# Performance work log

Measured on AMD Instinct MI355X. Metric: run time of the kernel, lower is better.

The kernel has to match this reference:

```python
import jax, jax.numpy as jnp
import numpy as np
import math

N_HEADS = 16
D_EFF = 64
ROPE_BASE = 500.0


def _rope(x, cos, sin):
    # x: (b, h, L, d_eff); cos/sin: (L, d_eff//2)
    x_even = x[..., 0::2]
    x_odd = x[..., 1::2]
    rot = jnp.stack([x_even * cos - x_odd * sin,
                     x_even * sin + x_odd * cos], axis=-1)
    return rot.reshape(x.shape)


def setup_inputs() -> dict:
    key = jax.random.key(0)
    ks = jax.random.split(key, 5)
    B, L, D = 1, 2048, 1024
    X = jax.random.normal(ks[0], (B, L, D), dtype=jnp.float32)
    # causal mask (1 = keep, 0 = masked), broadcastable to (B, h, L, L)
    mask = jnp.tril(jnp.ones((L, L), dtype=jnp.int32))[None, :, :]
    s = 1.0 / math.sqrt(D)
    Wq = jax.random.normal(ks[1], (D, D), dtype=jnp.float32) * s
    Wk = jax.random.normal(ks[2], (D, D), dtype=jnp.float32) * s
    Wv = jax.random.normal(ks[3], (D, D), dtype=jnp.float32) * s
    Wo = jax.random.normal(ks[4], (D, D), dtype=jnp.float32) * s
    return {"X": X, "mask": mask, "Wq": Wq, "Wk": Wk, "Wv": Wv, "Wo": Wo}


def reference(X, mask, Wq, Wk, Wv, Wo):
    b, L, d_model = X.shape
    h, d = N_HEADS, D_EFF
    d_full = h * d

    def split_heads(Y):
        return Y.reshape(b, L, h, d).transpose(0, 2, 1, 3)  # (b,h,L,d)

    Q = split_heads(X @ Wq)
    K = split_heads(X @ Wk)
    V = split_heads(X @ Wv)

    # interleaved RoPE, base 500
    inv_freq = 1.0 / (ROPE_BASE ** (jnp.arange(0, d, 2, dtype=jnp.float32) / d))
    freqs = jnp.arange(L, dtype=jnp.float32)[:, None] * inv_freq  # (L, d/2)
    cos, sin = jnp.cos(freqs), jnp.sin(freqs)
    Q = _rope(Q, cos, sin)
    K = _rope(K, cos, sin)

    S = jnp.einsum('bhqd,bhkd->bhqk', Q, K) / math.sqrt(d)
    S = jnp.where(mask[:, None, :, :] == 0, jnp.float32(-1e9), S)
    # NOTE: faithful to original torch code: softmax over the HEADS axis (dim=1)
    A = jax.nn.softmax(S, axis=1)
    Y = jnp.einsum('bhqk,bhkd->bhqd', A, V)
    Y = Y.transpose(0, 2, 1, 3).reshape(b, L, d_full)
    Y = Y @ Wo
    return Y * math.sqrt(d_model / d_full)
```

## Files before the change

kernel.cpp:

```cpp
#include <hip/hip_runtime.h>
#include <stdint.h>
#include <stddef.h>
#include <math.h>

typedef __attribute__((ext_vector_type(8))) short bf16x8;
typedef __attribute__((ext_vector_type(4))) short short4v;
typedef __attribute__((ext_vector_type(4))) float f32x4;

__device__ __forceinline__ short f2bf(float f) {
  union { float f; uint32_t u; } x; x.f = f;
  return (short)((x.u + 0x7fffu + ((x.u >> 16) & 1u)) >> 16);
}
__device__ __forceinline__ float bf2f(short s) {
  union { uint32_t u; float f; } x; x.u = ((uint32_t)(uint16_t)s) << 16;
  return x.f;
}
__device__ __forceinline__ uint32_t cvt_pk_bf16(float a, float b) {
  uint32_t r;
  asm("v_cvt_pk_bf16_f32 %0, %1, %2" : "=v"(r) : "v"(a), "v"(b));
  return r;
}

__device__ __forceinline__ void gload_lds16(const void* g, void* lds) {
  __builtin_amdgcn_global_load_lds(
      (const __attribute__((address_space(1))) void*)g,
      (__attribute__((address_space(3))) void*)lds, 16, 0, 0);
}

__global__ __launch_bounds__(256) void cast_b(const float* __restrict__ s,
                                              short* __restrict__ d) {
  int i4 = (blockIdx.x * 256 + threadIdx.x) * 4;
  float4 v = *(const float4*)&s[i4];
  short4v r = { f2bf(v.x), f2bf(v.y), f2bf(v.z), f2bf(v.w) };
  *(short4v*)&d[i4] = r;
}

__global__ __launch_bounds__(256) void reduce_y(const short* __restrict__ Ypc,
                                                const float* __restrict__ Cvs,
                                                short* __restrict__ o) {
  int q = blockIdx.x;
  int j = q >> 5, qr = q & 31;
  int col = threadIdx.x * 4;
  float a0 = Cvs[col + 0], a1 = Cvs[col + 1], a2 = Cvs[col + 2], a3 = Cvs[col + 3];
  int cf = (j - 2) >> 2;
  for (int c = 0; c <= cf; c++) {
    int slot = (c <= 7) ? (c + 8 * (j - 4 * c - 2)) : ((15 - c) + 8 * j);
    const short* p = Ypc + ((size_t)slot * 32 + qr) * 1024 + col;
    short4v v = *(const short4v*)p;
    a0 += bf2f(v[0]); a1 += bf2f(v[1]); a2 += bf2f(v[2]); a3 += bf2f(v[3]);
  }
  if ((j & 3) < 2) {
    int cp = j >> 2;
    int slot = (cp <= 7) ? (cp + 8 * (64 + (j & 3)))
                         : ((15 - cp) + 8 * (66 + (j & 3)));
    const short* p = Ypc + ((size_t)slot * 32 + qr) * 1024 + col;
    short4v v = *(const short4v*)p;
    a0 += bf2f(v[0]); a1 += bf2f(v[1]); a2 += bf2f(v[2]); a3 += bf2f(v[3]);
  }
  uint32_t u0 = cvt_pk_bf16(a0, a1), u1 = cvt_pk_bf16(a2, a3);
  short4v rr = { (short)u0, (short)(u0 >> 16), (short)u1, (short)(u1 >> 16) };
  *(short4v*)&o[(size_t)q * 1024 + col] = rr;
}

__global__ __launch_bounds__(256) void transW(const float* __restrict__ Wq,
                                              const float* __restrict__ Wk,
                                              const float* __restrict__ Wv,
                                              const float* __restrict__ Wo,
                                              short* __restrict__ WcatT,
                                              short* __restrict__ WoT) {
  int z = blockIdx.z;
  const float* src = (z == 0) ? Wq : (z == 1) ? Wk : (z == 2) ? Wv : Wo;
  short* dst = (z == 3) ? WoT : WcatT + (size_t)z * 1024 * 1024;
  __shared__ float tl[32][33];
  int tx = threadIdx.x & 31, ty = threadIdx.x >> 5;
  int kk0 = blockIdx.x * 32;
  int nn0 = blockIdx.y * 32;
#pragma unroll
  for (int j = 0; j < 4; j++)
    tl[ty + j * 8][tx] = src[(size_t)(kk0 + ty + j * 8) * 1024 + nn0 + tx];
  __syncthreads();
#pragma unroll
  for (int j = 0; j < 4; j++)
    dst[(size_t)(nn0 + ty + j * 8) * 1024 + kk0 + tx] = f2bf(tl[tx][ty + j * 8]);
}

__global__ __launch_bounds__(256) void transpose_v(const short* __restrict__ Vb,
                                                   short* __restrict__ Vt) {
  __shared__ short tv[64][72];
  int h = blockIdx.y, k0 = blockIdx.x * 64;
  int tid = threadIdx.x;
#pragma unroll
  for (int j = 0; j < 2; j++) {
    int idx = tid + j * 256;
    int row = idx >> 3, c = idx & 7;
    bf16x8 v = *(const bf16x8*)&Vb[((size_t)h * 2048 + k0 + row) * 64 + c * 8];
#pragma unroll
    for (int t = 0; t < 8; t++) tv[row][c * 8 + t] = v[t];
  }
  __syncthreads();
#pragma unroll
  for (int j = 0; j < 2; j++) {
    int idx = tid + j * 256;
    int d = idx >> 3, c = idx & 7;
    bf16x8 v;
#pragma unroll
    for (int t = 0; t < 8; t++) v[t] = tv[c * 8 + t][d];
    *(bf16x8*)&Vt[((size_t)h * 64 + d) * 2048 + k0 + c * 8] = v;
  }
}

__global__ __launch_bounds__(256) void vsum(const short* __restrict__ Vb,
                                            float* __restrict__ Cvs) {
  __shared__ float red[16][17];
  int h = blockIdx.x >> 2, dq = blockIdx.x & 3;
  int dl = threadIdx.x & 15, ks = threadIdx.x >> 4;
  int d = dq * 16 + dl;
  float acc = 0.f;
  const short* base = &Vb[((size_t)h * 2048 + ks * 128) * 64 + d];
#pragma unroll 8
  for (int k = 0; k < 128; k++) acc += bf2f(base[(size_t)k * 64]);
  red[dl][ks] = acc;
  __syncthreads();
  if (threadIdx.x < 16) {
    float sum = 0.f;
#pragma unroll
    for (int i = 0; i < 16; i++) sum += red[threadIdx.x][i];
    Cvs[h * 64 + dq * 16 + threadIdx.x] = sum * 0.0625f;
  }
}

template <int MODE>
__global__ __launch_bounds__(256, 2)
void gemm_kernel(const short* __restrict__ A, const short* __restrict__ B,
                 int N, int K, float* __restrict__ C,
                 short* __restrict__ Qb, short* __restrict__ Kb,
                 short* __restrict__ Vb) {
  __shared__ __attribute__((aligned(16))) short lga[128 * 64];
  __shared__ __attribute__((aligned(16))) short lgb[128 * 64];
  const int tid = threadIdx.x;
  const int lane = tid & 63;
  const int w = tid >> 6;
  const int l15 = lane & 15;
  const int quad = lane >> 4;
  const int wm = w >> 1, wn = w & 1;
  const int m0 = blockIdx.x * 128, n0 = blockIdx.y * 128;
  const int rsub = lane >> 3;
  const int cpos = lane & 7;

  f32x4 acc[4][4];
#pragma unroll
  for (int i = 0; i < 4; i++)
#pragma unroll
    for (int j = 0; j < 4; j++) acc[i][j] = (f32x4){0.f, 0.f, 0.f, 0.f};

  for (int kb = 0; kb < K; kb += 64) {
    __syncthreads();
#pragma unroll
    for (int j = 0; j < 4; j++) {
      int r = (w * 4 + j) * 8 + rsub;
      int kc = cpos ^ rsub;
      gload_lds16(A + (size_t)(m0 + r) * K + kb + kc * 8, &lga[(w * 4 + j) * 512]);
      gload_lds16(B + (size_t)(n0 + r) * K + kb + kc * 8, &lgb[(w * 4 + j) * 512]);
    }
    __syncthreads();
#pragma unroll
    for (int kk = 0; kk < 2; kk++) {
      bf16x8 af[4], bfr[4];
#pragma unroll
      for (int t = 0; t < 4; t++) {
        int row = wm * 64 + t * 16 + l15;
        int pc = (kk * 4 + quad) ^ (row & 7);
        af[t] = *(const bf16x8*)&lga[row * 64 + pc * 8];
        int rowb = wn * 64 + t * 16 + l15;
        int pcb = (kk * 4 + quad) ^ (rowb & 7);
        bfr[t] = *(const bf16x8*)&lgb[rowb * 64 + pcb * 8];
      }
#pragma unroll
      for (int mt = 0; mt < 4; mt++)
#pragma unroll
        for (int nt = 0; nt < 4; nt++)
          acc[mt][nt] = __builtin_amdgcn_mfma_f32_16x16x32_bf16(
              af[mt], bfr[nt], acc[mt][nt], 0, 0, 0);
    }
  }

  if (MODE == 0) {
#pragma unroll
    for (int mt = 0; mt < 4; mt++) {
      int q = m0 + wm * 64 + mt * 16 + quad * 4;
#pragma unroll
      for (int nt = 0; nt < 4; nt++) {
        int n = n0 + wn * 64 + nt * 16 + l15;
#pragma unroll
        for (int r = 0; r < 4; r++) C[(size_t)(q + r) * N + n] = acc[mt][nt][r];
      }
    }
  } else {
#pragma unroll
    for (int mt = 0; mt < 4; mt++) {
#pragma unroll
      for (int nt = 0; nt < 4; nt++) {
        int n = n0 + wn * 64 + nt * 16 + l15;
        int mat = n >> 10;
        int h = (n >> 6) & 15;
        int d = n & 63;
#pragma unroll
        for (int r = 0; r < 4; r++) {
          int q = m0 + wm * 64 + mt * 16 + quad * 4 + r;
          float v = acc[mt][nt][r];
          float o = __shfl_xor(v, 1, 64);
          if (mat < 2) {
            int i = d >> 1;
            float ang = (float)q * __builtin_exp2f(-(float)i * 0.2801807588956902f);
            float sn, cs;
            __sincosf(ang, &sn, &cs);
            float rv = (d & 1) ? (o * sn + v * cs) : (v * cs - o * sn);
            short* dst = (mat == 0) ? Qb : Kb;
            dst[((size_t)h * 2048 + q) * 64 + d] = f2bf(rv);
          } else {
            Vb[((size_t)h * 2048 + q) * 64 + d] = f2bf(v);
          }
        }
      }
    }
  }
}

__global__ __launch_bounds__(1024, 2)
void attn_kernel(const short* __restrict__ Qb, const short* __restrict__ Kb,
                 const short* __restrict__ Vt, short* __restrict__ Ypc) {
  __shared__ short Sb[16 * 32 * 72];
  const int tid = threadIdx.x;
  const int lane = tid & 63;
  const int h = tid >> 6;
  const int l15 = lane & 15, quad = lane >> 4;
  const int b = blockIdx.x;
  const int x = b & 7, s = b >> 3;
  int c, j, ng;
  const int n1 = 62 - 4 * x;
  if (s < n1)      { c = x;      j = 4 * x + 2 + s;        ng = 2; }
  else if (s < 64) { c = 15 - x; j = s;                    ng = 2; }
  else if (s < 66) { c = x;      j = 4 * x + (s - 64);     ng = 1; }
  else             { c = 15 - x; j = 60 - 4 * x + (s - 66); ng = 1; }
  const int q0 = j * 32;
  const int g0 = 2 * c;

  bf16x8 qf[2][2];
#pragma unroll
  for (int qs = 0; qs < 2; qs++)
#pragma unroll
    for (int cc = 0; cc < 2; cc++)
      qf[qs][cc] = *(const bf16x8*)&Qb[((size_t)h * 2048 + q0 + qs * 16 + l15) * 64 +
                                       cc * 32 + quad * 8];

  f32x4 yacc[2][4];
#pragma unroll
  for (int i = 0; i < 2; i++)
#pragma unroll
    for (int jj = 0; jj < 4; jj++) yacc[i][jj] = (f32x4){0.f, 0.f, 0.f, 0.f};

  for (int gi = 0; gi < ng; gi++) {
    const int k0 = (g0 + gi) * 64;
#pragma unroll
    for (int st = 0; st < 4; st++) {
      const short* kb = &Kb[((size_t)h * 2048 + k0 + st * 16 + l15) * 64 + quad * 8];
      bf16x8 kf0 = *(const bf16x8*)kb;
      bf16x8 kf1 = *(const bf16x8*)(kb + 32);
#pragma unroll
      for (int qs = 0; qs < 2; qs++) {
        f32x4 sa = (f32x4){0.f, 0.f, 0.f, 0.f};
        sa = __builtin_amdgcn_mfma_f32_16x16x32_bf16(qf[qs][0], kf0, sa, 0, 0, 0);
        sa = __builtin_amdgcn_mfma_f32_16x16x32_bf16(qf[qs][1], kf1, sa, 0, 0, 0);
        const float cs = 0.18033688011112042f;
        uint32_t u0 = cvt_pk_bf16(sa[0] * cs, sa[1] * cs);
        uint32_t u1 = cvt_pk_bf16(sa[2] * cs, sa[3] * cs);
        int rb = (h * 32 + qs * 16 + quad * 4) * 72 + st * 16 + l15;
        Sb[rb]       = (short)u0;
        Sb[rb + 72]  = (short)(u0 >> 16);
        Sb[rb + 144] = (short)u1;
        Sb[rb + 216] = (short)(u1 >> 16);
      }
    }
    __syncthreads();
#pragma unroll
    for (int pp = 0; pp < 2; pp++) {
      int p = tid + pp * 1024;
      int q = p >> 6, kl = p & 63;
      int base = q * 72 + kl;
      float t[16];
      float sum = 0.f;
#pragma unroll
      for (int hh = 0; hh < 16; hh++) {
        float e = __builtin_exp2f(bf2f(Sb[hh * 2304 + base]));
        t[hh] = e;
        sum += e;
      }
      bool msk = (k0 + kl) > (q0 + q);
      float rs = msk ? 0.f : 1.f / sum;
      float offv = msk ? 0.f : 0.0625f;
#pragma unroll
      for (int hh = 0; hh < 16; hh += 2) {
        uint32_t u = cvt_pk_bf16(t[hh] * rs - offv, t[hh + 1] * rs - offv);
        Sb[hh * 2304 + base]       = (short)u;
        Sb[(hh + 1) * 2304 + base] = (short)(u >> 16);
      }
    }
    __syncthreads();
#pragma unroll
    for (int kk = 0; kk < 2; kk++) {
      bf16x8 af0 = *(const bf16x8*)&Sb[(h * 32 + l15) * 72 + kk * 32 + quad * 8];
      bf16x8 af1 = *(const bf16x8*)&Sb[(h * 32 + 16 + l15) * 72 + kk * 32 + quad * 8];
#pragma unroll
      for (int nt = 0; nt < 4; nt++) {
        bf16x8 vf = *(const bf16x8*)&Vt[((size_t)h * 64 + nt * 16 + l15) * 2048 +
                                        k0 + kk * 32 + quad * 8];
        yacc[0][nt] = __builtin_amdgcn_mfma_f32_16x16x32_bf16(af0, vf, yacc[0][nt],
                                                              0, 0, 0);
        yacc[1][nt] = __builtin_amdgcn_mfma_f32_16x16x32_bf16(af1, vf, yacc[1][nt],
                                                              0, 0, 0);
      }
    }
    __syncthreads();
  }
  short* Y = Ypc + (size_t)b * 32 * 1024;
#pragma unroll
  for (int qs = 0; qs < 2; qs++) {
#pragma unroll
    for (int nt = 0; nt < 4; nt++) {
      int col = h * 64 + nt * 16 + l15;
#pragma unroll
      for (int rr = 0; rr < 4; rr++)
        Y[(size_t)(qs * 16 + quad * 4 + rr) * 1024 + col] = f2bf(yacc[qs][nt][rr]);
    }
  }
}

extern "C" void kernel_launch(void* const* d_in, const int* in_sizes, int n_in,
                              void* d_out, int out_size, void* d_ws, size_t ws_size,
                              hipStream_t stream) {
  (void)in_sizes; (void)n_in; (void)out_size; (void)ws_size;
  const float* X  = (const float*)d_in[0];
  const float* Wq = (const float*)d_in[2];
  const float* Wk = (const float*)d_in[3];
  const float* Wv = (const float*)d_in[4];
  const float* Wo = (const float*)d_in[5];
  char* ws = (char*)d_ws;
  const size_t MB = 1024 * 1024;
  short* Xbf   = (short*)(ws + 0);
  short* WcatT = (short*)(ws + 4 * MB);
  short* WoT   = (short*)(ws + 10 * MB);
  short* Qb    = (short*)(ws + 12 * MB);
  short* Kb    = (short*)(ws + 16 * MB);
  short* Vb    = (short*)(ws + 20 * MB);
  short* Vt    = (short*)(ws + 24 * MB);
  short* Ypc   = (short*)(ws + 28 * MB);
  float* Cvs   = (float*)(ws + 63 * MB);
  short* Ycbf  = Xbf;
  float* out   = (float*)d_out;

  cast_b<<<dim3(2048), dim3(256), 0, stream>>>(X, Xbf);
  transW<<<dim3(32, 32, 4), dim3(256), 0, stream>>>(Wq, Wk, Wv, Wo, WcatT, WoT);
  gemm_kernel<1><<<dim3(16, 24), dim3(256), 0, stream>>>(Xbf, WcatT, 3072, 1024,
                                                         nullptr, Qb, Kb, Vb);
  transpose_v<<<dim3(32, 16), dim3(256), 0, stream>>>(Vb, Vt);
  vsum<<<dim3(64), dim3(256), 0, stream>>>(Vb, Cvs);
  attn_kernel<<<dim3(544), dim3(1024), 0, stream>>>(Qb, Kb, Vt, Ypc);
  reduce_y<<<dim3(2048), dim3(256), 0, stream>>>(Ypc, Cvs, Ycbf);
  gemm_kernel<0><<<dim3(16, 8), dim3(256), 0, stream>>>(Ycbf, WoT, 1024, 1024,
                                                        out, nullptr, nullptr, nullptr);
}
```

Before: 212.3 us.

## Double-buffer attention score tiles and regroup work into 288 larger blocks

The attention kernel now gives each block up to four 64-key groups instead of two, which cuts the grid from 544 to 288 blocks and shrinks the partial-sum reduction. It uses two LDS score buffers so the PV MFMAs of the previous group overlap the QK of the next, and raises wave priority during PV. Softmax handles two key columns per thread with 32-bit LDS accesses. Doubling LDS and setting launch bounds to one block per CU lowers occupancy, and fewer, longer blocks can leave CUs unevenly loaded.

```diff
diff --git a/kernel.cpp b/kernel.cpp
--- a/kernel.cpp
+++ b/kernel.cpp
@@ -42,19 +42,16 @@
   int j = q >> 5, qr = q & 31;
   int col = threadIdx.x * 4;
   float a0 = Cvs[col + 0], a1 = Cvs[col + 1], a2 = Cvs[col + 2], a3 = Cvs[col + 3];
-  int cf = (j - 2) >> 2;
-  for (int c = 0; c <= cf; c++) {
-    int slot = (c <= 7) ? (c + 8 * (j - 4 * c - 2)) : ((15 - c) + 8 * j);
-    const short* p = Ypc + ((size_t)slot * 32 + qr) * 1024 + col;
-    short4v v = *(const short4v*)p;
-    a0 += bf2f(v[0]); a1 += bf2f(v[1]); a2 += bf2f(v[2]); a3 += bf2f(v[3]);
-  }
-  if ((j & 3) < 2) {
-    int cp = j >> 2;
-    int slot = (cp <= 7) ? (cp + 8 * (64 + (j & 3)))
-                         : ((15 - cp) + 8 * (66 + (j & 3)));
-    const short* p = Ypc + ((size_t)slot * 32 + qr) * 1024 + col;
-    short4v v = *(const short4v*)p;
+  int cmax = j >> 3;
+  for (int c = 0; c <= cmax; c++) {
+    int p, t;
+    if (c < 4) { p = c;     t = j - 8 * c; }
+    else       { p = 7 - c; t = j + 8; }
+    int x = 2 * p + (t & 1);
+    int s = 35 - (t >> 1);
+    int slot = x + 8 * s;
+    const short* pp = Ypc + ((size_t)slot * 32 + qr) * 1024 + col;
+    short4v v = *(const short4v*)pp;
     a0 += bf2f(v[0]); a1 += bf2f(v[1]); a2 += bf2f(v[2]); a3 += bf2f(v[3]);
   }
   uint32_t u0 = cvt_pk_bf16(a0, a1), u1 = cvt_pk_bf16(a2, a3);
@@ -226,24 +223,27 @@
   }
 }
 
-__global__ __launch_bounds__(1024, 2)
+__global__ __launch_bounds__(1024, 1)
 void attn_kernel(const short* __restrict__ Qb, const short* __restrict__ Kb,
                  const short* __restrict__ Vt, short* __restrict__ Ypc) {
-  __shared__ short Sb[16 * 32 * 72];
+  __shared__ short SbA[16 * 32 * 72];
+  __shared__ short SbB[16 * 32 * 72];
   const int tid = threadIdx.x;
   const int lane = tid & 63;
   const int h = tid >> 6;
   const int l15 = lane & 15, quad = lane >> 4;
   const int b = blockIdx.x;
-  const int x = b & 7, s = b >> 3;
-  int c, j, ng;
-  const int n1 = 62 - 4 * x;
-  if (s < n1)      { c = x;      j = 4 * x + 2 + s;        ng = 2; }
-  else if (s < 64) { c = 15 - x; j = s;                    ng = 2; }
-  else if (s < 66) { c = x;      j = 4 * x + (s - 64);     ng = 1; }
-  else             { c = 15 - x; j = 60 - 4 * x + (s - 66); ng = 1; }
+  const int x = b & 7;
+  const int p = x >> 1;
+  const int t = 2 * (35 - (b >> 3)) + (x & 1);
+  int c, j;
+  if (t < 64 - 8 * p) { c = p;     j = 8 * p + t; }
+  else                { c = 7 - p; j = t - 8; }
+  const int G = (j >> 1) + 1;
+  const int g0 = 4 * c;
+  int ngt = G - g0;
+  const int ng = (ngt > 4) ? 4 : ngt;
   const int q0 = j * 32;
-  const int g0 = 2 * c;
 
   bf16x8 qf[2][2];
 #pragma unroll
@@ -259,8 +259,7 @@
 #pragma unroll
     for (int jj = 0; jj < 4; jj++) yacc[i][jj] = (f32x4){0.f, 0.f, 0.f, 0.f};
 
-  for (int gi = 0; gi < ng; gi++) {
-    const int k0 = (g0 + gi) * 64;
+  auto QK = [&](short* Sb, int k0) {
 #pragma unroll
     for (int st = 0; st < 4; st++) {
       const short* kb = &Kb[((size_t)h * 2048 + k0 + st * 16 + l15) * 64 + quad * 8];
@@ -281,31 +280,9 @@
         Sb[rb + 216] = (short)(u1 >> 16);
       }
     }
-    __syncthreads();
-#pragma unroll
-    for (int pp = 0; pp < 2; pp++) {
-      int p = tid + pp * 1024;
-      int q = p >> 6, kl = p & 63;
-      int base = q * 72 + kl;
-      float t[16];
-      float sum = 0.f;
-#pragma unroll
-      for (int hh = 0; hh < 16; hh++) {
-        float e = __builtin_exp2f(bf2f(Sb[hh * 2304 + base]));
-        t[hh] = e;
-        sum += e;
-      }
-      bool msk = (k0 + kl) > (q0 + q);
-      float rs = msk ? 0.f : 1.f / sum;
-      float offv = msk ? 0.f : 0.0625f;
-#pragma unroll
-      for (int hh = 0; hh < 16; hh += 2) {
-        uint32_t u = cvt_pk_bf16(t[hh] * rs - offv, t[hh + 1] * rs - offv);
-        Sb[hh * 2304 + base]       = (short)u;
-        Sb[(hh + 1) * 2304 + base] = (short)(u >> 16);
-      }
-    }
-    __syncthreads();
+  };
+  auto PV = [&](const short* Sb, int k0) {
+    __builtin_amdgcn_s_setprio(1);
 #pragma unroll
     for (int kk = 0; kk < 2; kk++) {
       bf16x8 af0 = *(const bf16x8*)&Sb[(h * 32 + l15) * 72 + kk * 32 + quad * 8];
@@ -320,8 +297,48 @@
                                                               0, 0, 0);
       }
     }
+    __builtin_amdgcn_s_setprio(0);
+  };
+  auto SM = [&](short* Sb, int k0) {
+    int q = tid >> 5;
+    int kl2 = (tid & 31) * 2;
+    int base = q * 72 + kl2;
+    float t0[16], t1[16];
+    float s0 = 0.f, s1 = 0.f;
+#pragma unroll
+    for (int hh = 0; hh < 16; hh++) {
+      uint32_t u = *(const uint32_t*)&Sb[hh * 2304 + base];
+      float e0 = __builtin_exp2f(bf2f((short)u));
+      float e1 = __builtin_exp2f(bf2f((short)(u >> 16)));
+      t0[hh] = e0; t1[hh] = e1;
+      s0 += e0; s1 += e1;
+    }
+    bool m0 = (k0 + kl2)     > (q0 + q);
+    bool m1 = (k0 + kl2 + 1) > (q0 + q);
+    float rs0 = m0 ? 0.f : 1.f / s0;
+    float rs1 = m1 ? 0.f : 1.f / s1;
+    float o0 = m0 ? 0.f : 0.0625f;
+    float o1 = m1 ? 0.f : 0.0625f;
+#pragma unroll
+    for (int hh = 0; hh < 16; hh++) {
+      uint32_t w = cvt_pk_bf16(t0[hh] * rs0 - o0, t1[hh] * rs1 - o1);
+      *(uint32_t*)&Sb[hh * 2304 + base] = w;
+    }
+  };
+
+  int k0p = 0;
+  for (int gi = 0; gi < ng; gi++) {
+    const int k0 = (g0 + gi) * 64;
+    short* Sw = (gi & 1) ? SbB : SbA;
+    QK(Sw, k0);
+    if (gi > 0) PV((gi & 1) ? SbA : SbB, k0p);
     __syncthreads();
-  }
+    SM(Sw, k0);
+    __syncthreads();
+    k0p = k0;
+  }
+  PV(((ng - 1) & 1) ? SbB : SbA, k0p);
+
   short* Y = Ypc + (size_t)b * 32 * 1024;
 #pragma unroll
   for (int qs = 0; qs < 2; qs++) {
@@ -364,7 +381,7 @@
                                                          nullptr, Qb, Kb, Vb);
   transpose_v<<<dim3(32, 16), dim3(256), 0, stream>>>(Vb, Vt);
   vsum<<<dim3(64), dim3(256), 0, stream>>>(Vb, Cvs);
-  attn_kernel<<<dim3(544), dim3(1024), 0, stream>>>(Qb, Kb, Vt, Ypc);
+  attn_kernel<<<dim3(288), dim3(1024), 0, stream>>>(Qb, Kb, Vt, Ypc);
   reduce_y<<<dim3(2048), dim3(256), 0, stream>>>(Ypc, Cvs, Ycbf);
   gemm_kernel<0><<<dim3(16, 8), dim3(256), 0, stream>>>(Ycbf, WoT, 1024, 1024,
                                                         out, nullptr, nullptr, nullptr);
```

Measured after the change: 230.7 us. +8.7%, slower.
